# Kernel tuning notes

Measured on AMD Instinct MI355X. Metric: run time of the kernel, lower is better.

The kernel has to match this reference:

```python
import jax, jax.numpy as jnp
import numpy as np
import math

N_HEADS = 16
DIM = 1024
D_HEAD = DIM // N_HEADS
BS, QLEN = 2, 2048


def setup_inputs() -> dict:
    key = jax.random.key(0)
    ks = jax.random.split(key, 10)
    s = 0.02
    return {
        "input": jax.random.normal(ks[0], (BS, QLEN, DIM), dtype=jnp.float32),
        "mask": jnp.ones((BS, QLEN), dtype=jnp.int32),
        "q_w": jax.random.normal(ks[1], (DIM, DIM), dtype=jnp.float32) * s,
        "q_b": jax.random.normal(ks[2], (DIM,), dtype=jnp.float32) * s,
        "k_w": jax.random.normal(ks[3], (DIM, DIM), dtype=jnp.float32) * s,
        "k_b": jax.random.normal(ks[4], (DIM,), dtype=jnp.float32) * s,
        "v_w": jax.random.normal(ks[5], (DIM, DIM), dtype=jnp.float32) * s,
        "v_b": jax.random.normal(ks[6], (DIM,), dtype=jnp.float32) * s,
        "o_w": jax.random.normal(ks[7], (DIM, DIM), dtype=jnp.float32) * s,
        "o_b": jax.random.normal(ks[8], (DIM,), dtype=jnp.float32) * s,
    }


def _shape(x, bs):
    # (bs, len, dim) -> (bs, heads, len, d_head)
    return x.reshape(bs, -1, N_HEADS, D_HEAD).transpose(0, 2, 1, 3)


def reference(input, mask, q_w, q_b, k_w, k_b, v_w, v_b, o_w, o_b):
    bs, qlen, dim = input.shape
    # projections (torch Linear: x @ W^T + b)
    q = _shape(input @ q_w.T + q_b, bs)
    k = _shape(input @ k_w.T + k_b, bs)
    v = _shape(input @ v_w.T + v_b, bs)
    q = q / math.sqrt(D_HEAD)
    # scores: (bs, heads, qlen, klen)
    scores = jnp.einsum("bhqd,bhkd->bhqk", q, k)
    pad = (mask == 0)[:, None, None, :]  # (bs,1,1,klen)
    scores = jnp.where(pad, -jnp.inf, scores)
    weights = jax.nn.softmax(scores.astype(jnp.float32), axis=-1).astype(scores.dtype)
    # dropout p=0.0 (eval) -> identity
    context = jnp.einsum("bhqk,bhkd->bhqd", weights, v)
    context = context.transpose(0, 2, 1, 3).reshape(bs, qlen, dim)
    return context @ o_w.T + o_b
```

## Files before the change

### kernel.cpp

```cpp
#include <hip/hip_runtime.h>


#define BS    2
#define QLEN  2048
#define DIM   1024
#define NH    16
#define DH    64
#define MTOK  (BS * QLEN)

#define QSCALE 0.18033688011112042f

typedef __attribute__((ext_vector_type(8))) short short8;
typedef __attribute__((ext_vector_type(4))) float float4_t;
typedef __attribute__((ext_vector_type(4))) int   int4_t;

__device__ __forceinline__ ushort f2bf(float f) {
    unsigned u = __float_as_uint(f);
    return (ushort)((u + 0x7fffu + ((u >> 16) & 1u)) >> 16);
}
__device__ __forceinline__ short8 pack8(float4 a0, float4 a1) {
    short8 r;
    r[0] = (short)f2bf(a0.x); r[1] = (short)f2bf(a0.y);
    r[2] = (short)f2bf(a0.z); r[3] = (short)f2bf(a0.w);
    r[4] = (short)f2bf(a1.x); r[5] = (short)f2bf(a1.y);
    r[6] = (short)f2bf(a1.z); r[7] = (short)f2bf(a1.w);
    return r;
}

__device__ __forceinline__ void glds16(const void* g, void* l) {
    __builtin_amdgcn_global_load_lds(
        (const __attribute__((address_space(1))) unsigned int*)g,
        (__attribute__((address_space(3))) unsigned int*)l, 16, 0, 0);
}

__global__ __launch_bounds__(256) void conv_all(
    const float* __restrict__ x,  const float* __restrict__ qw,
    const float* __restrict__ kw, const float* __restrict__ vw,
    const float* __restrict__ ow,
    ushort* __restrict__ Xbf, ushort* __restrict__ Wbf)
{
    const int blk = blockIdx.x;
    const float* s; ushort* d; size_t base;
    if (blk < 4096)      { s = x;  d = Xbf;             base = (size_t)blk * 1024; }
    else if (blk < 5120) { s = qw; d = Wbf;             base = (size_t)(blk - 4096) * 1024; }
    else if (blk < 6144) { s = kw; d = Wbf + 1048576;   base = (size_t)(blk - 5120) * 1024; }
    else if (blk < 7168) { s = vw; d = Wbf + 2097152;   base = (size_t)(blk - 6144) * 1024; }
    else                 { s = ow; d = Wbf + 3145728;   base = (size_t)(blk - 7168) * 1024; }
    const size_t i = base + threadIdx.x * 4;
    float4 v = *(const float4*)(s + i);
    ushort4 o;
    o.x = f2bf(v.x); o.y = f2bf(v.y); o.z = f2bf(v.z); o.w = f2bf(v.w);
    *(ushort4*)(d + i) = o;
}

__global__ __launch_bounds__(256) void transpose_v(
    const ushort* __restrict__ Vrow, ushort* __restrict__ Vt)
{
    __shared__ ushort T[64][72];
    const int tid  = threadIdx.x;
    const int tile = blockIdx.x;
    const int bh   = blockIdx.y;
    const int b = bh >> 4, h = bh & 15;

    #pragma unroll
    for (int rep = 0; rep < 2; ++rep) {
        int ch = tid + rep * 256;
        int tok = ch >> 3, seg = ch & 7;
        uint4 v = *(const uint4*)(Vrow + (size_t)(b * QLEN + tile * 64 + tok) * DIM
                                        + h * DH + seg * 8);
        *(uint4*)&T[tok][seg * 8] = v;
    }
    __syncthreads();
    #pragma unroll
    for (int rep = 0; rep < 2; ++rep) {
        int ch = tid + rep * 256;
        int dim = ch >> 3, tseg = ch & 7;
        ushort t0 = T[tseg * 8 + 0][dim], t1 = T[tseg * 8 + 1][dim];
        ushort t2 = T[tseg * 8 + 2][dim], t3 = T[tseg * 8 + 3][dim];
        ushort t4 = T[tseg * 8 + 4][dim], t5 = T[tseg * 8 + 5][dim];
        ushort t6 = T[tseg * 8 + 6][dim], t7 = T[tseg * 8 + 7][dim];
        uint4 o;
        o.x = (unsigned)t0 | ((unsigned)t1 << 16);
        o.y = (unsigned)t2 | ((unsigned)t3 << 16);
        o.z = (unsigned)t4 | ((unsigned)t5 << 16);
        o.w = (unsigned)t6 | ((unsigned)t7 << 16);
        *(uint4*)(Vt + (size_t)bh * DH * QLEN + (size_t)dim * QLEN
                      + tile * 64 + tseg * 8) = o;
    }
}

__global__ __launch_bounds__(256) void gemm_m97(
    const ushort* __restrict__ A, const ushort* __restrict__ Bw,
    const float* __restrict__ bias0, const float* __restrict__ bias1,
    const float* __restrict__ bias2,
    ushort* __restrict__ outQ, ushort* __restrict__ outK, ushort* __restrict__ outV,
    float* __restrict__ outF,
    int N, int K, int mode)
{
    __shared__ ushort As[128 * 32];
    __shared__ ushort Bs[128 * 32];
    const int tid  = threadIdx.x;
    const int w    = tid >> 6;
    const int lane = tid & 63;
    const int r15  = lane & 15;
    const int quad = lane >> 4;
    const int nblk = N >> 7;
    const int brow = blockIdx.x / nblk;
    const int bcol = blockIdx.x - brow * nblk;
    const int wrow = (w >> 1) * 64;
    const int wcol = (w & 1) * 64;

    float4_t acc[4][4];
    #pragma unroll
    for (int i = 0; i < 4; ++i)
        #pragma unroll
        for (int j = 0; j < 4; ++j)
            acc[i][j] = (float4_t){0.f, 0.f, 0.f, 0.f};

    int ch0 = w * 64 + lane;
    int ch1 = ch0 + 256;
    const int row0 = ch0 >> 2, s0 = ch0 & 3, gk0 = s0 ^ ((row0 >> 1) & 3);
    const int row1 = ch1 >> 2, s1 = ch1 & 3, gk1 = s1 ^ ((row1 >> 1) & 3);

    const ushort* ga0 = A + (size_t)(brow * 128 + row0) * K + gk0 * 8;
    const ushort* ga1 = A + (size_t)(brow * 128 + row1) * K + gk1 * 8;
    const ushort* gb0 = Bw + (size_t)(bcol * 128 + row0) * K + gk0 * 8;
    const ushort* gb1 = Bw + (size_t)(bcol * 128 + row1) * K + gk1 * 8;

    for (int k0 = 0; k0 < K; k0 += 32) {
        __syncthreads();
        glds16(ga0 + k0, As + ch0 * 8);
        glds16(ga1 + k0, As + ch1 * 8);
        glds16(gb0 + k0, Bs + ch0 * 8);
        glds16(gb1 + k0, Bs + ch1 * 8);
        __syncthreads();

        short8 af[4], bf[4];
        #pragma unroll
        for (int ms = 0; ms < 4; ++ms) {
            int row = wrow + ms * 16 + r15;
            int s = quad ^ ((row >> 1) & 3);
            af[ms] = *(const short8*)&As[row * 32 + s * 8];
        }
        #pragma unroll
        for (int ns = 0; ns < 4; ++ns) {
            int row = wcol + ns * 16 + r15;
            int s = quad ^ ((row >> 1) & 3);
            bf[ns] = *(const short8*)&Bs[row * 32 + s * 8];
        }
        #pragma unroll
        for (int ms = 0; ms < 4; ++ms)
            #pragma unroll
            for (int ns = 0; ns < 4; ++ns)
                acc[ms][ns] = __builtin_amdgcn_mfma_f32_16x16x32_bf16(
                    af[ms], bf[ns], acc[ms][ns], 0, 0, 0);
    }

    #pragma unroll
    for (int ms = 0; ms < 4; ++ms) {
        const int rowg = brow * 128 + wrow + ms * 16 + quad * 4;
        #pragma unroll
        for (int ns = 0; ns < 4; ++ns) {
            const int colg = bcol * 128 + wcol + ns * 16 + r15;
            if (mode == 0) {
                if (colg < 1024) {
                    const float bb = bias0[colg];
                    #pragma unroll
                    for (int r = 0; r < 4; ++r)
                        outQ[(size_t)(rowg + r) * 1024 + colg] =
                            f2bf((acc[ms][ns][r] + bb) * QSCALE);
                } else if (colg < 2048) {
                    const float bb = bias1[colg - 1024];
                    #pragma unroll
                    for (int r = 0; r < 4; ++r)
                        outK[(size_t)(rowg + r) * 1024 + (colg - 1024)] =
                            f2bf(acc[ms][ns][r] + bb);
                } else {
                    const float bb = bias2[colg - 2048];
                    #pragma unroll
                    for (int r = 0; r < 4; ++r)
                        outV[(size_t)(rowg + r) * 1024 + (colg - 2048)] =
                            f2bf(acc[ms][ns][r] + bb);
                }
            } else {
                const float bb = bias0[colg];
                #pragma unroll
                for (int r = 0; r < 4; ++r)
                    outF[(size_t)(rowg + r) * 1024 + colg] = acc[ms][ns][r] + bb;
            }
        }
    }
}

__global__ __launch_bounds__(256) void gemm_f32in_bf16out(
    const float* __restrict__ X, const float* __restrict__ W,
    const float* __restrict__ B, ushort* __restrict__ Out,
    int M, int N, int K, float scale)
{
    const int lane = threadIdx.x & 63;
    const int wid  = (blockIdx.x * blockDim.x + threadIdx.x) >> 6;
    const int tilesN = N >> 4;
    const int tm = wid / tilesN;
    const int tn = wid - tm * tilesN;
    const int r15  = lane & 15;
    const int quad = lane >> 4;

    const float* xp = X + (size_t)(tm * 16 + r15) * K + quad * 8;
    const float* wp = W + (size_t)(tn * 16 + r15) * K + quad * 8;

    float4_t acc = {0.f, 0.f, 0.f, 0.f};
    for (int k0 = 0; k0 < K; k0 += 32) {
        float4 a0 = *(const float4*)(xp + k0);
        float4 a1 = *(const float4*)(xp + k0 + 4);
        float4 b0 = *(const float4*)(wp + k0);
        float4 b1 = *(const float4*)(wp + k0 + 4);
        acc = __builtin_amdgcn_mfma_f32_16x16x32_bf16(pack8(a0, a1), pack8(b0, b1), acc, 0, 0, 0);
    }
    const int col  = tn * 16 + r15;
    const float bias = B[col];
    const int row0 = tm * 16 + quad * 4;
    #pragma unroll
    for (int r = 0; r < 4; ++r)
        Out[(size_t)(row0 + r) * N + col] = f2bf((acc[r] + bias) * scale);
}

__global__ __launch_bounds__(256) void gemm_bf16in_f32out(
    const ushort* __restrict__ X, const float* __restrict__ W,
    const float* __restrict__ B, float* __restrict__ Out,
    int M, int N, int K)
{
    const int lane = threadIdx.x & 63;
    const int wid  = (blockIdx.x * blockDim.x + threadIdx.x) >> 6;
    const int tilesN = N >> 4;
    const int tm = wid / tilesN;
    const int tn = wid - tm * tilesN;
    const int r15  = lane & 15;
    const int quad = lane >> 4;

    const ushort* xp = X + (size_t)(tm * 16 + r15) * K + quad * 8;
    const float*  wp = W + (size_t)(tn * 16 + r15) * K + quad * 8;

    float4_t acc = {0.f, 0.f, 0.f, 0.f};
    for (int k0 = 0; k0 < K; k0 += 32) {
        short8 a = *(const short8*)(xp + k0);
        float4 b0 = *(const float4*)(wp + k0);
        float4 b1 = *(const float4*)(wp + k0 + 4);
        acc = __builtin_amdgcn_mfma_f32_16x16x32_bf16(a, pack8(b0, b1), acc, 0, 0, 0);
    }
    const int col  = tn * 16 + r15;
    const float bias = B[col];
    const int row0 = tm * 16 + quad * 4;
    #pragma unroll
    for (int r = 0; r < 4; ++r)
        Out[(size_t)(row0 + r) * N + col] = acc[r] + bias;
}

__global__ __launch_bounds__(256) void flash_attn(
    const ushort* __restrict__ Qb, const ushort* __restrict__ Kb,
    const ushort* __restrict__ Vt, const int* __restrict__ mask,
    ushort* __restrict__ Cb)
{
    __shared__ __align__(16) ushort Ks[2][64][64];
    __shared__ __align__(16) ushort Vs[2][64][64];
    __shared__ __align__(16) float  Mb[QLEN];

    const int tid  = threadIdx.x;
    const int w    = tid >> 6;
    const int lane = tid & 63;
    const int r15  = lane & 15;
    const int quad = lane >> 4;
    const int bh = blockIdx.y;
    const int b = bh >> 4, h = bh & 15;

    {
        const int4* m4 = (const int4*)(mask + b * QLEN);
        #pragma unroll
        for (int rep = 0; rep < 2; ++rep) {
            const int idx = tid + rep * 256;
            int4 mv = m4[idx];
            float4 o;
            o.x = mv.x ? 0.f : -INFINITY;
            o.y = mv.y ? 0.f : -INFINITY;
            o.z = mv.z ? 0.f : -INFINITY;
            o.w = mv.w ? 0.f : -INFINITY;
            *(float4*)&Mb[idx * 4] = o;
        }
    }

    const int qbase = blockIdx.x * 128 + w * 32;
    const ushort* qp = Qb + (size_t)(b * QLEN + qbase + r15) * DIM + h * DH + quad * 8;
    short8 qf[2][2];
    qf[0][0] = *(const short8*)(qp);
    qf[0][1] = *(const short8*)(qp + 32);
    qf[1][0] = *(const short8*)(qp + 16 * DIM);
    qf[1][1] = *(const short8*)(qp + 16 * DIM + 32);

    const ushort* kg = Kb + (size_t)b * QLEN * DIM + h * DH;
    const ushort* vg = Vt + (size_t)bh * DH * QLEN;

    const int a0 = tid >> 3, seg = tid & 7;
    const int krow0 = (((a0 & 7) >> 2) << 4) + (((a0 >> 3) & 3) << 2) + (a0 & 3);
    const int sK = (seg ^ (krow0 & 7)) << 3;
    const int sV = (seg ^ (a0 & 7)) << 3;
    const int xq = (quad ^ (r15 & 7)) << 3;

    float4_t o[2][4];
    float4_t ol[2];
    #pragma unroll
    for (int rg = 0; rg < 2; ++rg) {
        ol[rg] = (float4_t){0.f, 0.f, 0.f, 0.f};
        #pragma unroll
        for (int ds = 0; ds < 4; ++ds)
            o[rg][ds] = (float4_t){0.f, 0.f, 0.f, 0.f};
    }
    short8 ones8;
    #pragma unroll
    for (int i = 0; i < 8; ++i) ones8[i] = (short)0x3F80;

    uint4 kr0 = *(const uint4*)(kg + (size_t)(a0     ) * DIM + seg * 8);
    uint4 kr1 = *(const uint4*)(kg + (size_t)(a0 + 32) * DIM + seg * 8);
    uint4 vr0 = *(const uint4*)(vg + (size_t)(a0     ) * QLEN + seg * 8);
    uint4 vr1 = *(const uint4*)(vg + (size_t)(a0 + 32) * QLEN + seg * 8);
    *(uint4*)&Ks[0][krow0     ][sK] = kr0;
    *(uint4*)&Ks[0][krow0 + 32][sK] = kr1;
    *(uint4*)&Vs[0][a0        ][sV] = vr0;
    *(uint4*)&Vs[0][a0 + 32   ][sV] = vr1;
    __syncthreads();

    int p = 0;
    for (int kt = 0; kt < QLEN; kt += 64) {
        const bool more = (kt + 64 < QLEN);
        if (more) {
            kr0 = *(const uint4*)(kg + (size_t)(kt + 64 + a0     ) * DIM + seg * 8);
            kr1 = *(const uint4*)(kg + (size_t)(kt + 64 + a0 + 32) * DIM + seg * 8);
            vr0 = *(const uint4*)(vg + (size_t)(a0     ) * QLEN + kt + 64 + seg * 8);
            vr1 = *(const uint4*)(vg + (size_t)(a0 + 32) * QLEN + kt + 64 + seg * 8);
        }

        int pk[4][2][2];
        #pragma unroll
        for (int ks = 0; ks < 4; ++ks) {
            const ushort* krow = &Ks[p][ks * 16 + r15][0];
            short8 kf0 = *(const short8*)(krow + xq);
            short8 kf1 = *(const short8*)(krow + (xq ^ 32));
            const float4 mb = *(const float4*)&Mb[kt + ((ks >> 1) << 5)
                                                   + (quad << 3) + ((ks & 1) << 2)];
            #pragma unroll
            for (int rg = 0; rg < 2; ++rg) {
                float4_t s = {0.f, 0.f, 0.f, 0.f};
                s = __builtin_amdgcn_mfma_f32_16x16x32_bf16(kf0, qf[rg][0], s, 0, 0, 0);
                s = __builtin_amdgcn_mfma_f32_16x16x32_bf16(kf1, qf[rg][1], s, 0, 0, 0);
                unsigned u0 = __float_as_uint(__builtin_amdgcn_exp2f(s[0] + mb.x));
                unsigned u1 = __float_as_uint(__builtin_amdgcn_exp2f(s[1] + mb.y));
                unsigned u2 = __float_as_uint(__builtin_amdgcn_exp2f(s[2] + mb.z));
                unsigned u3 = __float_as_uint(__builtin_amdgcn_exp2f(s[3] + mb.w));
                pk[ks][rg][0] = __builtin_amdgcn_perm(u1, u0, 0x07060302);
                pk[ks][rg][1] = __builtin_amdgcn_perm(u3, u2, 0x07060302);
            }
        }

        #pragma unroll
        for (int ck = 0; ck < 2; ++ck) {
            short8 vf[4];
            #pragma unroll
            for (int ds = 0; ds < 4; ++ds)
                vf[ds] = *(const short8*)(&Vs[p][ds * 16 + r15][0] + (xq ^ (ck << 5)));
            #pragma unroll
            for (int rg = 0; rg < 2; ++rg) {
                int4_t pfi = { pk[2 * ck][rg][0], pk[2 * ck][rg][1],
                               pk[2 * ck + 1][rg][0], pk[2 * ck + 1][rg][1] };
                short8 pf = __builtin_bit_cast(short8, pfi);
                #pragma unroll
                for (int ds = 0; ds < 4; ++ds)
                    o[rg][ds] = __builtin_amdgcn_mfma_f32_16x16x32_bf16(
                        pf, vf[ds], o[rg][ds], 0, 0, 0);
                ol[rg] = __builtin_amdgcn_mfma_f32_16x16x32_bf16(
                    pf, ones8, ol[rg], 0, 0, 0);
            }
        }

        if (more) {
            *(uint4*)&Ks[p ^ 1][krow0     ][sK] = kr0;
            *(uint4*)&Ks[p ^ 1][krow0 + 32][sK] = kr1;
            *(uint4*)&Vs[p ^ 1][a0        ][sV] = vr0;
            *(uint4*)&Vs[p ^ 1][a0 + 32   ][sV] = vr1;
        }
        __syncthreads();
        p ^= 1;
    }

    #pragma unroll
    for (int rg = 0; rg < 2; ++rg) {
        #pragma unroll
        for (int r = 0; r < 4; ++r) {
            const float ir = 1.f / fmaxf(ol[rg][r], 1e-30f);
            const size_t rb = (size_t)(b * QLEN + qbase + rg * 16 + quad * 4 + r) * DIM
                              + h * DH;
            Cb[rb +  0 + r15] = f2bf(o[rg][0][r] * ir);
            Cb[rb + 16 + r15] = f2bf(o[rg][1][r] * ir);
            Cb[rb + 32 + r15] = f2bf(o[rg][2][r] * ir);
            Cb[rb + 48 + r15] = f2bf(o[rg][3][r] * ir);
        }
    }
}

extern "C" void kernel_launch(void* const* d_in, const int* in_sizes, int n_in,
                              void* d_out, int out_size, void* d_ws, size_t ws_size,
                              hipStream_t stream)
{
    const float* x    = (const float*)d_in[0];
    const int*   mask = (const int*)d_in[1];
    const float* q_w  = (const float*)d_in[2];
    const float* q_b  = (const float*)d_in[3];
    const float* k_w  = (const float*)d_in[4];
    const float* k_b  = (const float*)d_in[5];
    const float* v_w  = (const float*)d_in[6];
    const float* v_b  = (const float*)d_in[7];
    const float* o_w  = (const float*)d_in[8];
    const float* o_b  = (const float*)d_in[9];
    float* out = (float*)d_out;

    const size_t SEG = (size_t)MTOK * DIM;
    ushort* Qbf = (ushort*)d_out;
    ushort* Xbf = Qbf + SEG;
    ushort* Kb  = (ushort*)d_ws;
    ushort* Vrow = Kb + SEG;
    ushort* Cb   = Vrow;
    ushort* Vt  = Vrow + SEG;
    ushort* Wbf = Vt + SEG;

    const bool big = ws_size >= (size_t)32 * 1024 * 1024;

    if (big) {
        conv_all<<<8192, 256, 0, stream>>>(x, q_w, k_w, v_w, o_w, Xbf, Wbf);
        gemm_m97<<<(MTOK / 128) * (3072 / 128), 256, 0, stream>>>(
            Xbf, Wbf, q_b, k_b, v_b, Qbf, Kb, Vrow, nullptr, 3072, DIM, 0);
    } else {
        const int tiles   = (MTOK / 16) * (DIM / 16);
        const int gblocks = tiles / 4;
        gemm_f32in_bf16out<<<gblocks, 256, 0, stream>>>(x, q_w, q_b, Qbf, MTOK, DIM, DIM, QSCALE);
        gemm_f32in_bf16out<<<gblocks, 256, 0, stream>>>(x, k_w, k_b, Kb,  MTOK, DIM, DIM, 1.0f);
        gemm_f32in_bf16out<<<gblocks, 256, 0, stream>>>(x, v_w, v_b, Vrow, MTOK, DIM, DIM, 1.0f);
    }

    transpose_v<<<dim3(QLEN / 64, BS * NH), 256, 0, stream>>>(Vrow, Vt);

    flash_attn<<<dim3(QLEN / 128, BS * NH), 256, 0, stream>>>(Qbf, Kb, Vt, mask, Cb);

    if (big) {
        gemm_m97<<<(MTOK / 128) * (DIM / 128), 256, 0, stream>>>(
            Cb, Wbf + 3 * (size_t)(DIM * DIM), o_b, nullptr, nullptr,
            nullptr, nullptr, nullptr, out, DIM, DIM, 1);
    } else {
        const int tiles = (MTOK / 16) * (DIM / 16);
        gemm_bf16in_f32out<<<tiles / 4, 256, 0, stream>>>(Cb, o_w, o_b, out, MTOK, DIM, DIM);
    }
}
```

Measured before the change: 210.3 us.

## Fuse V transpose into QKV GEMM epilogue, split O-proj tiles, skip mask adds

The QKV projection GEMM now writes V straight into the per-head transposed layout, which removes the separate transpose_v kernel and its extra round trip through memory. The output projection gets its own 128x64-tile kernel, doubling the block count for better occupancy on the smaller N=1024 GEMM. Flash attention precomputes a per-64-key-tile flag for whether any key in the tile is padded, and skips the mask load and add when none is. The transposed V store is only 4 elements wide per lane, so the writes are poorly coalesced.

```diff
diff --git a/kernel.cpp b/kernel.cpp
--- a/kernel.cpp
+++ b/kernel.cpp
@@ -89,13 +89,11 @@
     }
 }
 
-__global__ __launch_bounds__(256) void gemm_m97(
+__global__ __launch_bounds__(256) void gemm_qkv(
     const ushort* __restrict__ A, const ushort* __restrict__ Bw,
     const float* __restrict__ bias0, const float* __restrict__ bias1,
     const float* __restrict__ bias2,
-    ushort* __restrict__ outQ, ushort* __restrict__ outK, ushort* __restrict__ outV,
-    float* __restrict__ outF,
-    int N, int K, int mode)
+    ushort* __restrict__ outQ, ushort* __restrict__ outK, ushort* __restrict__ outVt)
 {
     __shared__ ushort As[128 * 32];
     __shared__ ushort Bs[128 * 32];
@@ -104,11 +102,12 @@
     const int lane = tid & 63;
     const int r15  = lane & 15;
     const int quad = lane >> 4;
-    const int nblk = N >> 7;
+    const int nblk = 3072 >> 7;
     const int brow = blockIdx.x / nblk;
     const int bcol = blockIdx.x - brow * nblk;
     const int wrow = (w >> 1) * 64;
     const int wcol = (w & 1) * 64;
+    const int K = DIM;
 
     float4_t acc[4][4];
     #pragma unroll
@@ -162,32 +161,105 @@
         #pragma unroll
         for (int ns = 0; ns < 4; ++ns) {
             const int colg = bcol * 128 + wcol + ns * 16 + r15;
-            if (mode == 0) {
-                if (colg < 1024) {
-                    const float bb = bias0[colg];
-                    #pragma unroll
-                    for (int r = 0; r < 4; ++r)
-                        outQ[(size_t)(rowg + r) * 1024 + colg] =
-                            f2bf((acc[ms][ns][r] + bb) * QSCALE);
-                } else if (colg < 2048) {
-                    const float bb = bias1[colg - 1024];
-                    #pragma unroll
-                    for (int r = 0; r < 4; ++r)
-                        outK[(size_t)(rowg + r) * 1024 + (colg - 1024)] =
-                            f2bf(acc[ms][ns][r] + bb);
-                } else {
-                    const float bb = bias2[colg - 2048];
-                    #pragma unroll
-                    for (int r = 0; r < 4; ++r)
-                        outV[(size_t)(rowg + r) * 1024 + (colg - 2048)] =
-                            f2bf(acc[ms][ns][r] + bb);
-                }
-            } else {
+            if (colg < 1024) {
                 const float bb = bias0[colg];
                 #pragma unroll
                 for (int r = 0; r < 4; ++r)
-                    outF[(size_t)(rowg + r) * 1024 + colg] = acc[ms][ns][r] + bb;
+                    outQ[(size_t)(rowg + r) * 1024 + colg] =
+                        f2bf((acc[ms][ns][r] + bb) * QSCALE);
+            } else if (colg < 2048) {
+                const float bb = bias1[colg - 1024];
+                #pragma unroll
+                for (int r = 0; r < 4; ++r)
+                    outK[(size_t)(rowg + r) * 1024 + (colg - 1024)] =
+                        f2bf(acc[ms][ns][r] + bb);
+            } else {
+                const int vcol = colg - 2048;
+                const int hh = vcol >> 6, dd = vcol & 63;
+                const float bb = bias2[vcol];
+                const int bidx = rowg >> 11;
+                const int tloc = rowg & 2047;
+                ushort4 o4;
+                o4.x = f2bf(acc[ms][ns][0] + bb);
+                o4.y = f2bf(acc[ms][ns][1] + bb);
+                o4.z = f2bf(acc[ms][ns][2] + bb);
+                o4.w = f2bf(acc[ms][ns][3] + bb);
+                *(ushort4*)&outVt[((size_t)(bidx * 16 + hh) * 64 + dd) * QLEN + tloc] = o4;
             }
+        }
+    }
+}
+
+__global__ __launch_bounds__(256) void gemm_o(
+    const ushort* __restrict__ A, const ushort* __restrict__ Bw,
+    const float* __restrict__ bias, float* __restrict__ Out)
+{
+    __shared__ ushort As[128 * 32];
+    __shared__ ushort Bs[64 * 32];
+    const int tid  = threadIdx.x;
+    const int w    = tid >> 6;
+    const int lane = tid & 63;
+    const int r15  = lane & 15;
+    const int quad = lane >> 4;
+    const int brow = blockIdx.x >> 4;
+    const int bcol = blockIdx.x & 15;
+    const int wrow = w * 32;
+    const int K = DIM;
+
+    float4_t acc[2][4];
+    #pragma unroll
+    for (int i = 0; i < 2; ++i)
+        #pragma unroll
+        for (int j = 0; j < 4; ++j)
+            acc[i][j] = (float4_t){0.f, 0.f, 0.f, 0.f};
+
+    const int chA0 = w * 64 + lane, chA1 = chA0 + 256;
+    const int rA0 = chA0 >> 2, sA0 = chA0 & 3, gkA0 = sA0 ^ ((rA0 >> 1) & 3);
+    const int rA1 = chA1 >> 2, sA1 = chA1 & 3, gkA1 = sA1 ^ ((rA1 >> 1) & 3);
+    const int rB  = tid >> 2,  sB  = tid & 3,  gkB  = sB  ^ ((rB  >> 1) & 3);
+
+    const ushort* ga0 = A + (size_t)(brow * 128 + rA0) * K + gkA0 * 8;
+    const ushort* ga1 = A + (size_t)(brow * 128 + rA1) * K + gkA1 * 8;
+    const ushort* gb  = Bw + (size_t)(bcol * 64 + rB) * K + gkB * 8;
+
+    for (int k0 = 0; k0 < K; k0 += 32) {
+        __syncthreads();
+        glds16(ga0 + k0, As + chA0 * 8);
+        glds16(ga1 + k0, As + chA1 * 8);
+        glds16(gb + k0,  Bs + tid * 8);
+        __syncthreads();
+
+        short8 af[2], bf[4];
+        #pragma unroll
+        for (int ms = 0; ms < 2; ++ms) {
+            int row = wrow + ms * 16 + r15;
+            int s = quad ^ ((row >> 1) & 3);
+            af[ms] = *(const short8*)&As[row * 32 + s * 8];
+        }
+        #pragma unroll
+        for (int ns = 0; ns < 4; ++ns) {
+            int row = ns * 16 + r15;
+            int s = quad ^ ((row >> 1) & 3);
+            bf[ns] = *(const short8*)&Bs[row * 32 + s * 8];
+        }
+        #pragma unroll
+        for (int ms = 0; ms < 2; ++ms)
+            #pragma unroll
+            for (int ns = 0; ns < 4; ++ns)
+                acc[ms][ns] = __builtin_amdgcn_mfma_f32_16x16x32_bf16(
+                    af[ms], bf[ns], acc[ms][ns], 0, 0, 0);
+    }
+
+    #pragma unroll
+    for (int ms = 0; ms < 2; ++ms) {
+        const int rowg = brow * 128 + wrow + ms * 16 + quad * 4;
+        #pragma unroll
+        for (int ns = 0; ns < 4; ++ns) {
+            const int colg = bcol * 64 + ns * 16 + r15;
+            const float bb = bias[colg];
+            #pragma unroll
+            for (int r = 0; r < 4; ++r)
+                Out[(size_t)(rowg + r) * 1024 + colg] = acc[ms][ns][r] + bb;
         }
     }
 }
@@ -263,6 +335,7 @@
     __shared__ __align__(16) ushort Ks[2][64][64];
     __shared__ __align__(16) ushort Vs[2][64][64];
     __shared__ __align__(16) float  Mb[QLEN];
+    __shared__ int Kflag[QLEN / 64];
 
     const int tid  = threadIdx.x;
     const int w    = tid >> 6;
@@ -327,6 +400,18 @@
     *(uint4*)&Vs[0][a0 + 32   ][sV] = vr1;
     __syncthreads();
 
+    if (tid < QLEN / 64) {
+        const float4* m4 = (const float4*)&Mb[tid * 64];
+        float acc = 0.f;
+        #pragma unroll
+        for (int i = 0; i < 16; ++i) {
+            float4 v = m4[i];
+            acc += v.x + v.y + v.z + v.w;
+        }
+        Kflag[tid] = (acc < -1e30f) ? 1 : 0;
+    }
+    __syncthreads();
+
     int p = 0;
     for (int kt = 0; kt < QLEN; kt += 64) {
         const bool more = (kt + 64 < QLEN);
@@ -336,6 +421,7 @@
             vr0 = *(const uint4*)(vg + (size_t)(a0     ) * QLEN + kt + 64 + seg * 8);
             vr1 = *(const uint4*)(vg + (size_t)(a0 + 32) * QLEN + kt + 64 + seg * 8);
         }
+        const int hasmask = Kflag[kt >> 6];
 
         int pk[4][2][2];
         #pragma unroll
@@ -343,17 +429,25 @@
             const ushort* krow = &Ks[p][ks * 16 + r15][0];
             short8 kf0 = *(const short8*)(krow + xq);
             short8 kf1 = *(const short8*)(krow + (xq ^ 32));
-            const float4 mb = *(const float4*)&Mb[kt + ((ks >> 1) << 5)
-                                                   + (quad << 3) + ((ks & 1) << 2)];
             #pragma unroll
             for (int rg = 0; rg < 2; ++rg) {
                 float4_t s = {0.f, 0.f, 0.f, 0.f};
                 s = __builtin_amdgcn_mfma_f32_16x16x32_bf16(kf0, qf[rg][0], s, 0, 0, 0);
                 s = __builtin_amdgcn_mfma_f32_16x16x32_bf16(kf1, qf[rg][1], s, 0, 0, 0);
-                unsigned u0 = __float_as_uint(__builtin_amdgcn_exp2f(s[0] + mb.x));
-                unsigned u1 = __float_as_uint(__builtin_amdgcn_exp2f(s[1] + mb.y));
-                unsigned u2 = __float_as_uint(__builtin_amdgcn_exp2f(s[2] + mb.z));
-                unsigned u3 = __float_as_uint(__builtin_amdgcn_exp2f(s[3] + mb.w));
+                unsigned u0, u1, u2, u3;
+                if (hasmask) {
+                    const float4 mb = *(const float4*)&Mb[kt + ((ks >> 1) << 5)
+                                                           + (quad << 3) + ((ks & 1) << 2)];
+                    u0 = __float_as_uint(__builtin_amdgcn_exp2f(s[0] + mb.x));
+                    u1 = __float_as_uint(__builtin_amdgcn_exp2f(s[1] + mb.y));
+                    u2 = __float_as_uint(__builtin_amdgcn_exp2f(s[2] + mb.z));
+                    u3 = __float_as_uint(__builtin_amdgcn_exp2f(s[3] + mb.w));
+                } else {
+                    u0 = __float_as_uint(__builtin_amdgcn_exp2f(s[0]));
+                    u1 = __float_as_uint(__builtin_amdgcn_exp2f(s[1]));
+                    u2 = __float_as_uint(__builtin_amdgcn_exp2f(s[2]));
+                    u3 = __float_as_uint(__builtin_amdgcn_exp2f(s[3]));
+                }
                 pk[ks][rg][0] = __builtin_amdgcn_perm(u1, u0, 0x07060302);
                 pk[ks][rg][1] = __builtin_amdgcn_perm(u3, u2, 0x07060302);
             }
@@ -424,35 +518,29 @@
     ushort* Qbf = (ushort*)d_out;
     ushort* Xbf = Qbf + SEG;
     ushort* Kb  = (ushort*)d_ws;
-    ushort* Vrow = Kb + SEG;
-    ushort* Cb   = Vrow;
-    ushort* Vt  = Vrow + SEG;
+    ushort* Cb  = Kb + SEG;
+    ushort* Vt  = Cb + SEG;
     ushort* Wbf = Vt + SEG;
 
     const bool big = ws_size >= (size_t)32 * 1024 * 1024;
 
     if (big) {
         conv_all<<<8192, 256, 0, stream>>>(x, q_w, k_w, v_w, o_w, Xbf, Wbf);
-        gemm_m97<<<(MTOK / 128) * (3072 / 128), 256, 0, stream>>>(
-            Xbf, Wbf, q_b, k_b, v_b, Qbf, Kb, Vrow, nullptr, 3072, DIM, 0);
+        gemm_qkv<<<(MTOK / 128) * (3072 / 128), 256, 0, stream>>>(
+            Xbf, Wbf, q_b, k_b, v_b, Qbf, Kb, Vt);
+
+        flash_attn<<<dim3(QLEN / 128, BS * NH), 256, 0, stream>>>(Qbf, Kb, Vt, mask, Cb);
+
+        gemm_o<<<(MTOK / 128) * (DIM / 64), 256, 0, stream>>>(
+            Cb, Wbf + 3 * (size_t)(DIM * DIM), o_b, out);
     } else {
         const int tiles   = (MTOK / 16) * (DIM / 16);
         const int gblocks = tiles / 4;
         gemm_f32in_bf16out<<<gblocks, 256, 0, stream>>>(x, q_w, q_b, Qbf, MTOK, DIM, DIM, QSCALE);
         gemm_f32in_bf16out<<<gblocks, 256, 0, stream>>>(x, k_w, k_b, Kb,  MTOK, DIM, DIM, 1.0f);
-        gemm_f32in_bf16out<<<gblocks, 256, 0, stream>>>(x, v_w, v_b, Vrow, MTOK, DIM, DIM, 1.0f);
-    }
-
-    transpose_v<<<dim3(QLEN / 64, BS * NH), 256, 0, stream>>>(Vrow, Vt);
-
-    flash_attn<<<dim3(QLEN / 128, BS * NH), 256, 0, stream>>>(Qbf, Kb, Vt, mask, Cb);
-
-    if (big) {
-        gemm_m97<<<(MTOK / 128) * (DIM / 128), 256, 0, stream>>>(
-            Cb, Wbf + 3 * (size_t)(DIM * DIM), o_b, nullptr, nullptr,
-            nullptr, nullptr, nullptr, out, DIM, DIM, 1);
-    } else {
-        const int tiles = (MTOK / 16) * (DIM / 16);
+        gemm_f32in_bf16out<<<gblocks, 256, 0, stream>>>(x, v_w, v_b, Cb,  MTOK, DIM, DIM, 1.0f);
+        transpose_v<<<dim3(QLEN / 64, BS * NH), 256, 0, stream>>>(Cb, Vt);
+        flash_attn<<<dim3(QLEN / 128, BS * NH), 256, 0, stream>>>(Qbf, Kb, Vt, mask, Cb);
         gemm_bf16in_f32out<<<tiles / 4, 256, 0, stream>>>(Cb, o_w, o_b, out, MTOK, DIM, DIM);
     }
 }
```

After: 216.8 us. 1.03x slower.
